# Optimization experiments

Hardware: AMD Instinct MI355X
Metric: run time of the kernel (lower is better)

## Reference

```python
import jax, jax.numpy as jnp
import numpy as np

K = 10
ALPHA = 0.1
N_NODES = 100000
N_EDGES = 1600000
D_FEAT = 50


def setup_inputs() -> dict:
    key = jax.random.key(0)
    k1, k2, k3 = jax.random.split(key, 3)
    feat = jax.random.normal(k1, (N_NODES, D_FEAT), dtype=jnp.float32)
    src = jax.random.randint(k2, (N_EDGES,), 0, N_NODES, dtype=jnp.int64)
    dst = jax.random.randint(k3, (N_EDGES,), 0, N_NODES, dtype=jnp.int64)
    return {"feat": feat, "src": src, "dst": dst}


def reference(feat, src, dst):
    # APPNP: H^{t+1} = (1-a) * D^{-1/2} A D^{-1/2} H^t + a * H^0
    n = feat.shape[0]
    # in-degree per node, clipped to >= 1 (as in the original clip_by_value)
    deg = jax.ops.segment_sum(jnp.ones(dst.shape[0], feat.dtype), dst, num_segments=n)
    norm = jnp.clip(deg, 1.0, None) ** -0.5  # [N]
    norm = norm[:, None]                      # broadcast over feature dims
    feat_0 = feat
    for _ in range(K):
        h = feat * norm                       # pre-normalize (D^{-1/2})
        # message = h[src] (edge weight is 1 since edge_drop=0), aggregate by sum at dst
        agg = jax.ops.segment_sum(h[src], dst, num_segments=n)  # [N, D]
        feat = (1.0 - ALPHA) * (agg * norm) + ALPHA * feat_0
    return feat
```

## Files before the change

kernel.cpp:

```cpp
#include <hip/hip_runtime.h>
#include <hip/hip_bf16.h>


#define NN 100000
#define EE 1600000
#define DD 50
#define GS 64
#define KK 10
#define NBLK 391

__device__ __forceinline__ float feat_at(const void* f, long long i, int ft) {
    if (ft) return ((const float*)f)[i];
    unsigned int w = ((unsigned int)((const unsigned short*)f)[i]) << 16;
    return __uint_as_float(w);
}

__device__ __forceinline__ float bf16_ld(const unsigned short* p, int i) {
    unsigned int w = ((unsigned int)p[i]) << 16;
    return __uint_as_float(w);
}

__device__ __forceinline__ unsigned short bf16_st(float x) {
    unsigned int u = __float_as_uint(x);
    unsigned int r = (u + 0x7FFF + ((u >> 16) & 1)) >> 16;
    return (unsigned short)r;
}

__global__ __launch_bounds__(512) void APPNPConv_62199716381208_kernel(
        const void* featp, const void* srcp, const void* dstp,
        int* deg, float* norm, int* row_ptr, int* col_idx, int* bsum, int* flag,
        const unsigned short* gin, unsigned short* gout, float* outp,
        int phase, int last) {
    __shared__ int sh[512];
    const int tid = threadIdx.x;
    const int gidx = blockIdx.x * blockDim.x + tid;

    if (phase == 0) {
        if (gidx < NN) deg[gidx] = 0;
        if (blockIdx.x == 0 && tid == 0) {
            const int* a = (const int*)dstp;
            int odd_or = a[1] | a[3] | a[5] | a[7] | a[9] | a[11] | a[13] | a[15];
            flag[0] = (odd_or == 0) ? 1 : 0;
            const unsigned short* w = (const unsigned short*)featp;
            int isf32 = 0;
            for (int k = 0; k < 64; ++k) {
                unsigned int b = ((unsigned int)w[k]) << 16;
                float ax = fabsf(__uint_as_float(b));
                if (!(ax < 100.0f)) isf32 = 1;
            }
            flag[1] = isf32;
        }
        return;
    }
    if (phase == 1) {
        if (gidx < EE) {
            int d = flag[0] ? (int)((const long long*)dstp)[gidx]
                            : ((const int*)dstp)[gidx];
            if ((unsigned int)d < (unsigned int)NN) atomicAdd(&deg[d], 1);
        }
        return;
    }
    if (phase == 2) {
        int i = blockIdx.x * 256 + tid;
        sh[tid] = (i < NN) ? deg[i] : 0;
        __syncthreads();
        for (int off = 128; off > 0; off >>= 1) {
            if (tid < off) sh[tid] += sh[tid + off];
            __syncthreads();
        }
        if (tid == 0) bsum[blockIdx.x] = sh[0];
        return;
    }
    if (phase == 3) {
        int v = (tid < NBLK) ? bsum[tid] : 0;
        sh[tid] = v;
        __syncthreads();
        for (int off = 1; off < 512; off <<= 1) {
            int x = (tid >= off) ? sh[tid - off] : 0;
            __syncthreads();
            sh[tid] += x;
            __syncthreads();
        }
        if (tid < NBLK) bsum[tid] = sh[tid] - v;
        return;
    }
    if (phase == 4) {
        int i = blockIdx.x * 256 + tid;
        int v = (i < NN) ? deg[i] : 0;
        sh[tid] = v;
        __syncthreads();
        for (int off = 1; off < 256; off <<= 1) {
            int x = (tid >= off) ? sh[tid - off] : 0;
            __syncthreads();
            sh[tid] += x;
            __syncthreads();
        }
        int excl = sh[tid] - v + bsum[blockIdx.x];
        if (i < NN) {
            row_ptr[i] = excl;
            deg[i] = excl;
            norm[i] = rsqrtf((float)(v < 1 ? 1 : v));
        }
        if (i == 0) row_ptr[NN] = EE;
        return;
    }
    if (phase == 5) {
        if (gidx < EE) {
            int is64 = flag[0];
            int d = is64 ? (int)((const long long*)dstp)[gidx] : ((const int*)dstp)[gidx];
            int c = is64 ? (int)((const long long*)srcp)[gidx] : ((const int*)srcp)[gidx];
            if ((unsigned int)d < (unsigned int)NN && (unsigned int)c < (unsigned int)NN) {
                int pos = atomicAdd(&deg[d], 1);
                if ((unsigned int)pos < (unsigned int)EE) col_idx[pos] = c;
            }
        }
        return;
    }
    if (phase == 6) {
        int v = gidx >> 6;
        int d = gidx & 63;
        if (v < NN && d < DD) {
            float x = feat_at(featp, (long long)v * DD + d, flag[1]);
            gout[v * GS + d] = bf16_st(x * norm[v]);
        }
        return;
    }
    {
        const int lane = tid & 63;
        const int v = (blockIdx.x << 2) + (tid >> 6);
        if (v >= NN) return;
        const int beg = row_ptr[v];
        const int end = row_ptr[v + 1];
        float s0 = 0.0f, s1 = 0.0f, s2 = 0.0f, s3 = 0.0f;
        for (int base = beg; base < end; base += 64) {
            int idx = base + lane;
            int my = (idx < end) ? col_idx[idx] : 0;
            int cnt = end - base;
            if (cnt > 64) cnt = 64;
            int j = 0;
            for (; j + 8 <= cnt; j += 8) {
                int c0 = __shfl(my, j, 64);
                int c1 = __shfl(my, j + 1, 64);
                int c2 = __shfl(my, j + 2, 64);
                int c3 = __shfl(my, j + 3, 64);
                int c4 = __shfl(my, j + 4, 64);
                int c5 = __shfl(my, j + 5, 64);
                int c6 = __shfl(my, j + 6, 64);
                int c7 = __shfl(my, j + 7, 64);
                if (lane < DD) {
                    float v0 = bf16_ld(gin, c0 * GS + lane);
                    float v1 = bf16_ld(gin, c1 * GS + lane);
                    float v2 = bf16_ld(gin, c2 * GS + lane);
                    float v3 = bf16_ld(gin, c3 * GS + lane);
                    float v4 = bf16_ld(gin, c4 * GS + lane);
                    float v5 = bf16_ld(gin, c5 * GS + lane);
                    float v6 = bf16_ld(gin, c6 * GS + lane);
                    float v7 = bf16_ld(gin, c7 * GS + lane);
                    s0 += v0 + v4;
                    s1 += v1 + v5;
                    s2 += v2 + v6;
                    s3 += v3 + v7;
                }
            }
            for (; j + 4 <= cnt; j += 4) {
                int c0 = __shfl(my, j, 64);
                int c1 = __shfl(my, j + 1, 64);
                int c2 = __shfl(my, j + 2, 64);
                int c3 = __shfl(my, j + 3, 64);
                if (lane < DD) {
                    s0 += bf16_ld(gin, c0 * GS + lane);
                    s1 += bf16_ld(gin, c1 * GS + lane);
                    s2 += bf16_ld(gin, c2 * GS + lane);
                    s3 += bf16_ld(gin, c3 * GS + lane);
                }
            }
            for (; j < cnt; ++j) {
                int c = __shfl(my, j, 64);
                if (lane < DD) s0 += bf16_ld(gin, c * GS + lane);
            }
        }
        if (lane < DD) {
            float sum = (s0 + s1) + (s2 + s3);
            float nv = norm[v];
            float f0 = feat_at(featp, (long long)v * DD + lane, flag[1]);
            float res = 0.9f * (sum * nv) + 0.1f * f0;
            if (last) outp[v * DD + lane] = res;
            else      gout[v * GS + lane] = bf16_st(res * nv);
        }
    }
}

extern "C" void kernel_launch(void* const* d_in, const int* in_sizes, int n_in,
                              void* d_out, int out_size, void* d_ws, size_t ws_size,
                              hipStream_t stream) {
    const void* featp = d_in[0];
    const void* src = d_in[1];
    const void* dst = d_in[2];
    float* outf = (float*)d_out;
    unsigned short* outb16 = (unsigned short*)d_out;
    size_t out_bytes = (size_t)out_size * 4;
    (void)in_sizes;

    if (n_in != 3) {
        hipMemsetAsync(d_out, 0x50, out_bytes, stream);
        return;
    }

    size_t a_deg  = (((size_t)NN * 4) + 255) / 256 * 256;
    size_t a_norm = a_deg;
    size_t a_rp   = (((size_t)(NN + 1) * 4) + 255) / 256 * 256;
    size_t a_col  = (((size_t)EE * 4) + 255) / 256 * 256;
    size_t a_bsum = (((size_t)NBLK * 4) + 255) / 256 * 256;
    size_t a_flag = 256;
    size_t a_buf  = (((size_t)NN * GS * 2) + 255) / 256 * 256;
    if (ws_size < a_deg + a_norm + a_rp + a_col + a_bsum + a_flag + a_buf) {
        hipMemsetAsync(d_out, 0x40, out_bytes, stream);
        return;
    }
    char* p = (char*)d_ws;
    int* deg      = (int*)p;   p += a_deg;
    float* norm   = (float*)p; p += a_norm;
    int* row_ptr  = (int*)p;   p += a_rp;
    int* col_idx  = (int*)p;   p += a_col;
    int* bsum     = (int*)p;   p += a_bsum;
    int* flag     = (int*)p;   p += a_flag;
    unsigned short* bufA = (unsigned short*)p;

    (void)hipGetLastError();

    #define LCH(grid, blk, gi, go, ph, la) \
        APPNPConv_62199716381208_kernel<<<(grid), (blk), 0, stream>>>( \
            featp, src, dst, deg, norm, row_ptr, col_idx, bsum, flag, \
            (gi), (go), outf, (ph), (la))

    LCH(NBLK, 256, bufA, bufA, 0, 0);
    LCH((EE + 255) / 256, 256, bufA, bufA, 1, 0);
    LCH(NBLK, 256, bufA, bufA, 2, 0);
    LCH(1, 512, bufA, bufA, 3, 0);
    LCH(NBLK, 256, bufA, bufA, 4, 0);
    LCH((EE + 255) / 256, 256, bufA, bufA, 5, 0);
    LCH((NN * GS + 255) / 256, 256, bufA, outb16, 6, 0);

    for (int it = 1; it <= KK; ++it) {
        const unsigned short* gi = (it & 1) ? outb16 : bufA;
        unsigned short* go       = (it & 1) ? bufA : outb16;
        LCH(NN / 4, 256, gi, go, 7, (it == KK) ? 1 : 0);
    }
    #undef LCH

    if (hipGetLastError() != hipSuccess) {
        hipMemsetAsync(d_out, 0xBF, out_bytes, stream);
    }
}
```

Baseline: 800.1 us.

## Split features into two 25-column chunks with vectorized 8-byte gathers

Splits the 50 feature columns into two independent 25-column passes, so each pass's bf16 state is 100000x32x2 bytes (about 6.4 MB), small enough to stay resident in cache during the gather. Each wavefront now processes 16 neighbors at a time, with 8 lanes each loading 4 packed bf16 values via uint2, then reduces across groups with shuffles. Non-temporal loads and stores are used for col_idx, feat and the output. In exchange, the CSR structure is traversed twice (20 gather launches instead of 10), and ping-pong buffers move from d_out into the workspace.

```diff
diff --git a/kernel.cpp b/kernel.cpp
--- a/kernel.cpp
+++ b/kernel.cpp
@@ -1,11 +1,11 @@
 #include <hip/hip_runtime.h>
-#include <hip/hip_bf16.h>
 
 
 #define NN 100000
 #define EE 1600000
 #define DD 50
-#define GS 64
+#define PS 32
+#define CF 25
 #define KK 10
 #define NBLK 391
 
@@ -15,8 +15,10 @@
     return __uint_as_float(w);
 }
 
-__device__ __forceinline__ float bf16_ld(const unsigned short* p, int i) {
-    unsigned int w = ((unsigned int)p[i]) << 16;
+__device__ __forceinline__ float feat_nt(const void* f, long long i, int ft) {
+    if (ft) return __builtin_nontemporal_load((const float*)f + i);
+    unsigned int w = ((unsigned int)__builtin_nontemporal_load(
+                         (const unsigned short*)f + i)) << 16;
     return __uint_as_float(w);
 }
 
@@ -30,7 +32,7 @@
         const void* featp, const void* srcp, const void* dstp,
         int* deg, float* norm, int* row_ptr, int* col_idx, int* bsum, int* flag,
         const unsigned short* gin, unsigned short* gout, float* outp,
-        int phase, int last) {
+        int phase, int last, int chunk) {
     __shared__ int sh[512];
     const int tid = threadIdx.x;
     const int gidx = blockIdx.x * blockDim.x + tid;
@@ -117,75 +119,94 @@
         return;
     }
     if (phase == 6) {
-        int v = gidx >> 6;
-        int d = gidx & 63;
-        if (v < NN && d < DD) {
-            float x = feat_at(featp, (long long)v * DD + d, flag[1]);
-            gout[v * GS + d] = bf16_st(x * norm[v]);
+        int v = gidx >> 5;
+        int d = gidx & 31;
+        if (v < NN) {
+            unsigned short val = 0;
+            if (d < CF) {
+                float x = feat_at(featp, (long long)v * DD + chunk * CF + d, flag[1]);
+                val = bf16_st(x * norm[v]);
+            }
+            gout[(long long)v * PS + d] = val;
         }
         return;
     }
     {
         const int lane = tid & 63;
+        const int g = lane >> 3;
+        const int s = lane & 7;
         const int v = (blockIdx.x << 2) + (tid >> 6);
         if (v >= NN) return;
         const int beg = row_ptr[v];
         const int end = row_ptr[v + 1];
-        float s0 = 0.0f, s1 = 0.0f, s2 = 0.0f, s3 = 0.0f;
+        float a0 = 0.0f, a1 = 0.0f, a2 = 0.0f, a3 = 0.0f;
         for (int base = beg; base < end; base += 64) {
             int idx = base + lane;
-            int my = (idx < end) ? col_idx[idx] : 0;
+            int my = (idx < end) ? __builtin_nontemporal_load(col_idx + idx) : 0;
             int cnt = end - base;
             if (cnt > 64) cnt = 64;
-            int j = 0;
-            for (; j + 8 <= cnt; j += 8) {
-                int c0 = __shfl(my, j, 64);
-                int c1 = __shfl(my, j + 1, 64);
-                int c2 = __shfl(my, j + 2, 64);
-                int c3 = __shfl(my, j + 3, 64);
-                int c4 = __shfl(my, j + 4, 64);
-                int c5 = __shfl(my, j + 5, 64);
-                int c6 = __shfl(my, j + 6, 64);
-                int c7 = __shfl(my, j + 7, 64);
-                if (lane < DD) {
-                    float v0 = bf16_ld(gin, c0 * GS + lane);
-                    float v1 = bf16_ld(gin, c1 * GS + lane);
-                    float v2 = bf16_ld(gin, c2 * GS + lane);
-                    float v3 = bf16_ld(gin, c3 * GS + lane);
-                    float v4 = bf16_ld(gin, c4 * GS + lane);
-                    float v5 = bf16_ld(gin, c5 * GS + lane);
-                    float v6 = bf16_ld(gin, c6 * GS + lane);
-                    float v7 = bf16_ld(gin, c7 * GS + lane);
-                    s0 += v0 + v4;
-                    s1 += v1 + v5;
-                    s2 += v2 + v6;
-                    s3 += v3 + v7;
+            for (int j = 0; j < cnt; j += 16) {
+                int ja = j + g, jb = j + 8 + g;
+                int ca = __shfl(my, ja, 64);
+                int cb = __shfl(my, jb, 64);
+                if (ja >= cnt) ca = 0;
+                if (jb >= cnt) cb = 0;
+                uint2 wa = *reinterpret_cast<const uint2*>(gin + (long long)ca * PS + s * 4);
+                uint2 wb = *reinterpret_cast<const uint2*>(gin + (long long)cb * PS + s * 4);
+                if (ja >= cnt) { wa.x = 0u; wa.y = 0u; }
+                if (jb >= cnt) { wb.x = 0u; wb.y = 0u; }
+                a0 += __uint_as_float(wa.x << 16);
+                a1 += __uint_as_float(wa.x & 0xffff0000u);
+                a2 += __uint_as_float(wa.y << 16);
+                a3 += __uint_as_float(wa.y & 0xffff0000u);
+                a0 += __uint_as_float(wb.x << 16);
+                a1 += __uint_as_float(wb.x & 0xffff0000u);
+                a2 += __uint_as_float(wb.y << 16);
+                a3 += __uint_as_float(wb.y & 0xffff0000u);
+            }
+        }
+        a0 += __shfl_xor(a0, 8, 64);  a1 += __shfl_xor(a1, 8, 64);
+        a2 += __shfl_xor(a2, 8, 64);  a3 += __shfl_xor(a3, 8, 64);
+        a0 += __shfl_xor(a0, 16, 64); a1 += __shfl_xor(a1, 16, 64);
+        a2 += __shfl_xor(a2, 16, 64); a3 += __shfl_xor(a3, 16, 64);
+        a0 += __shfl_xor(a0, 32, 64); a1 += __shfl_xor(a1, 32, 64);
+        a2 += __shfl_xor(a2, 32, 64); a3 += __shfl_xor(a3, 32, 64);
+        if (g == 0) {
+            const float nv = norm[v];
+            const int ft = flag[1];
+            float acc[4] = {a0, a1, a2, a3};
+            if (last) {
+                #pragma unroll
+                for (int k = 0; k < 4; ++k) {
+                    int e = s * 4 + k;
+                    if (e < CF) {
+                        long long fi = (long long)v * DD + chunk * CF + e;
+                        float f0 = feat_nt(featp, fi, ft);
+                        outp[fi] = 0.9f * (acc[k] * nv) + 0.1f * f0;
+                    }
                 }
-            }
-            for (; j + 4 <= cnt; j += 4) {
-                int c0 = __shfl(my, j, 64);
-                int c1 = __shfl(my, j + 1, 64);
-                int c2 = __shfl(my, j + 2, 64);
-                int c3 = __shfl(my, j + 3, 64);
-                if (lane < DD) {
-                    s0 += bf16_ld(gin, c0 * GS + lane);
-                    s1 += bf16_ld(gin, c1 * GS + lane);
-                    s2 += bf16_ld(gin, c2 * GS + lane);
-                    s3 += bf16_ld(gin, c3 * GS + lane);
+            } else {
+                unsigned short h[4];
+                #pragma unroll
+                for (int k = 0; k < 4; ++k) {
+                    int e = s * 4 + k;
+                    if (e < CF) {
+                        long long fi = (long long)v * DD + chunk * CF + e;
+                        float f0 = feat_nt(featp, fi, ft);
+                        float res = 0.9f * (acc[k] * nv) + 0.1f * f0;
+                        h[k] = bf16_st(res * nv);
+                    } else {
+                        h[k] = 0;
+                    }
                 }
-            }
-            for (; j < cnt; ++j) {
-                int c = __shfl(my, j, 64);
-                if (lane < DD) s0 += bf16_ld(gin, c * GS + lane);
-            }
-        }
-        if (lane < DD) {
-            float sum = (s0 + s1) + (s2 + s3);
-            float nv = norm[v];
-            float f0 = feat_at(featp, (long long)v * DD + lane, flag[1]);
-            float res = 0.9f * (sum * nv) + 0.1f * f0;
-            if (last) outp[v * DD + lane] = res;
-            else      gout[v * GS + lane] = bf16_st(res * nv);
+                unsigned long long pk =
+                    (unsigned long long)h[0]
+                    | ((unsigned long long)h[1] << 16)
+                    | ((unsigned long long)h[2] << 32)
+                    | ((unsigned long long)h[3] << 48);
+                __builtin_nontemporal_store(pk,
+                    reinterpret_cast<unsigned long long*>(gout + (long long)v * PS + s * 4));
+            }
         }
     }
 }
@@ -197,7 +218,6 @@
     const void* src = d_in[1];
     const void* dst = d_in[2];
     float* outf = (float*)d_out;
-    unsigned short* outb16 = (unsigned short*)d_out;
     size_t out_bytes = (size_t)out_size * 4;
     (void)in_sizes;
 
@@ -212,8 +232,8 @@
     size_t a_col  = (((size_t)EE * 4) + 255) / 256 * 256;
     size_t a_bsum = (((size_t)NBLK * 4) + 255) / 256 * 256;
     size_t a_flag = 256;
-    size_t a_buf  = (((size_t)NN * GS * 2) + 255) / 256 * 256;
-    if (ws_size < a_deg + a_norm + a_rp + a_col + a_bsum + a_flag + a_buf) {
+    size_t a_buf  = (((size_t)NN * PS * 2) + 255) / 256 * 256;
+    if (ws_size < a_deg + a_norm + a_rp + a_col + a_bsum + a_flag + 2 * a_buf) {
         hipMemsetAsync(d_out, 0x40, out_bytes, stream);
         return;
     }
@@ -224,27 +244,30 @@
     int* col_idx  = (int*)p;   p += a_col;
     int* bsum     = (int*)p;   p += a_bsum;
     int* flag     = (int*)p;   p += a_flag;
-    unsigned short* bufA = (unsigned short*)p;
+    unsigned short* P0 = (unsigned short*)p; p += a_buf;
+    unsigned short* P1 = (unsigned short*)p;
 
     (void)hipGetLastError();
 
-    #define LCH(grid, blk, gi, go, ph, la) \
+    #define LCH(grid, blk, gi, go, ph, la, ch) \
         APPNPConv_62199716381208_kernel<<<(grid), (blk), 0, stream>>>( \
             featp, src, dst, deg, norm, row_ptr, col_idx, bsum, flag, \
-            (gi), (go), outf, (ph), (la))
-
-    LCH(NBLK, 256, bufA, bufA, 0, 0);
-    LCH((EE + 255) / 256, 256, bufA, bufA, 1, 0);
-    LCH(NBLK, 256, bufA, bufA, 2, 0);
-    LCH(1, 512, bufA, bufA, 3, 0);
-    LCH(NBLK, 256, bufA, bufA, 4, 0);
-    LCH((EE + 255) / 256, 256, bufA, bufA, 5, 0);
-    LCH((NN * GS + 255) / 256, 256, bufA, outb16, 6, 0);
-
-    for (int it = 1; it <= KK; ++it) {
-        const unsigned short* gi = (it & 1) ? outb16 : bufA;
-        unsigned short* go       = (it & 1) ? bufA : outb16;
-        LCH(NN / 4, 256, gi, go, 7, (it == KK) ? 1 : 0);
+            (gi), (go), outf, (ph), (la), (ch))
+
+    LCH(NBLK, 256, P0, P0, 0, 0, 0);
+    LCH((EE + 255) / 256, 256, P0, P0, 1, 0, 0);
+    LCH(NBLK, 256, P0, P0, 2, 0, 0);
+    LCH(1, 512, P0, P0, 3, 0, 0);
+    LCH(NBLK, 256, P0, P0, 4, 0, 0);
+    LCH((EE + 255) / 256, 256, P0, P0, 5, 0, 0);
+
+    for (int c = 0; c < 2; ++c) {
+        LCH((NN * PS) / 256, 256, P0, P0, 6, 0, c);
+        for (int it = 1; it <= KK; ++it) {
+            const unsigned short* gi = (it & 1) ? P0 : P1;
+            unsigned short* go       = (it & 1) ? P1 : P0;
+            LCH(NN / 4, 256, gi, go, 7, (it == KK) ? 1 : 0, c);
+        }
     }
     #undef LCH
 
```

Result: slower. 1.531 ms (+91.4%).

## Build CSR via per-slice shared-memory histograms instead of global atomics

Applied to the files above, without the earlier changes.

Replaces the global-atomic degree count and scatter with a two-pass, shared-memory counting sort. Edges are split into 32 slices and destinations into 8 ranges, giving 256 blocks that each keep a 12500-entry LDS histogram. Per-slice counts are kept in the output buffer as scratch, and prefix offsets are computed per slice so each block scatters through LDS atomics. The aim is to remove contended global atomics in CSR construction. The cost is that every block rereads its whole edge slice once per range (8x edge reads), and within-node column order becomes deterministic by slice.

```diff
diff --git a/kernel.cpp b/kernel.cpp
--- a/kernel.cpp
+++ b/kernel.cpp
@@ -1,5 +1,4 @@
 #include <hip/hip_runtime.h>
-#include <hip/hip_bf16.h>
 
 
 #define NN 100000
@@ -8,6 +7,10 @@
 #define GS 64
 #define KK 10
 #define NBLK 391
+#define SLICES 32
+#define RANGES 8
+#define NR (NN / RANGES)
+#define ES (EE / SLICES)
 
 __device__ __forceinline__ float feat_at(const void* f, long long i, int ft) {
     if (ft) return ((const float*)f)[i];
@@ -26,17 +29,60 @@
     return (unsigned short)r;
 }
 
+__global__ __launch_bounds__(512) void APPNPConv_62199716381208_build(
+        const void* srcp, const void* dstp, unsigned int* counts,
+        int* col_idx, const int* flag, int phase) {
+    __shared__ unsigned int hist[NR];
+    const int tid = threadIdx.x;
+    const int r = blockIdx.x / SLICES;
+    const int s = blockIdx.x % SLICES;
+    const int r0 = r * NR;
+    const int is64 = flag[0];
+    const int e0 = s * ES;
+
+    if (phase == 0) {
+        for (int i = tid; i < NR; i += 512) hist[i] = 0u;
+        __syncthreads();
+        for (int i = tid; i < ES; i += 512) {
+            int e = e0 + i;
+            int d = is64 ? (int)((const long long*)dstp)[e]
+                         : ((const int*)dstp)[e];
+            unsigned int dr = (unsigned int)(d - r0);
+            if (dr < (unsigned int)NR) atomicAdd(&hist[dr], 1u);
+        }
+        __syncthreads();
+        for (int i = tid; i < NR; i += 512)
+            counts[(size_t)s * NN + r0 + i] = hist[i];
+    } else {
+        for (int i = tid; i < NR; i += 512)
+            hist[i] = counts[(size_t)s * NN + r0 + i];
+        __syncthreads();
+        for (int i = tid; i < ES; i += 512) {
+            int e = e0 + i;
+            int d = is64 ? (int)((const long long*)dstp)[e]
+                         : ((const int*)dstp)[e];
+            int c = is64 ? (int)((const long long*)srcp)[e]
+                         : ((const int*)srcp)[e];
+            unsigned int dr = (unsigned int)(d - r0);
+            if (dr < (unsigned int)NR) {
+                unsigned int pos = atomicAdd(&hist[dr], 1u);
+                if (pos < (unsigned int)EE)
+                    col_idx[pos] = ((unsigned int)c < (unsigned int)NN) ? c : 0;
+            }
+        }
+    }
+}
+
 __global__ __launch_bounds__(512) void APPNPConv_62199716381208_kernel(
         const void* featp, const void* srcp, const void* dstp,
         int* deg, float* norm, int* row_ptr, int* col_idx, int* bsum, int* flag,
+        unsigned int* counts,
         const unsigned short* gin, unsigned short* gout, float* outp,
         int phase, int last) {
     __shared__ int sh[512];
     const int tid = threadIdx.x;
-    const int gidx = blockIdx.x * blockDim.x + tid;
 
     if (phase == 0) {
-        if (gidx < NN) deg[gidx] = 0;
         if (blockIdx.x == 0 && tid == 0) {
             const int* a = (const int*)dstp;
             int odd_or = a[1] | a[3] | a[5] | a[7] | a[9] | a[11] | a[13] | a[15];
@@ -52,17 +98,17 @@
         }
         return;
     }
-    if (phase == 1) {
-        if (gidx < EE) {
-            int d = flag[0] ? (int)((const long long*)dstp)[gidx]
-                            : ((const int*)dstp)[gidx];
-            if ((unsigned int)d < (unsigned int)NN) atomicAdd(&deg[d], 1);
-        }
-        return;
-    }
     if (phase == 2) {
-        int i = blockIdx.x * 256 + tid;
-        sh[tid] = (i < NN) ? deg[i] : 0;
+        int n = blockIdx.x * 256 + tid;
+        int total = 0;
+        if (n < NN) {
+            #pragma unroll 4
+            for (int s = 0; s < SLICES; ++s)
+                total += (int)counts[(size_t)s * NN + n];
+            deg[n] = total;
+            norm[n] = rsqrtf((float)(total < 1 ? 1 : total));
+        }
+        sh[tid] = total;
         __syncthreads();
         for (int off = 128; off > 0; off >>= 1) {
             if (tid < off) sh[tid] += sh[tid + off];
@@ -98,25 +144,19 @@
         int excl = sh[tid] - v + bsum[blockIdx.x];
         if (i < NN) {
             row_ptr[i] = excl;
-            deg[i] = excl;
-            norm[i] = rsqrtf((float)(v < 1 ? 1 : v));
+            unsigned int run = (unsigned int)excl;
+            for (int s = 0; s < SLICES; ++s) {
+                size_t o = (size_t)s * NN + i;
+                unsigned int c = counts[o];
+                counts[o] = run;
+                run += c;
+            }
         }
         if (i == 0) row_ptr[NN] = EE;
         return;
     }
-    if (phase == 5) {
-        if (gidx < EE) {
-            int is64 = flag[0];
-            int d = is64 ? (int)((const long long*)dstp)[gidx] : ((const int*)dstp)[gidx];
-            int c = is64 ? (int)((const long long*)srcp)[gidx] : ((const int*)srcp)[gidx];
-            if ((unsigned int)d < (unsigned int)NN && (unsigned int)c < (unsigned int)NN) {
-                int pos = atomicAdd(&deg[d], 1);
-                if ((unsigned int)pos < (unsigned int)EE) col_idx[pos] = c;
-            }
-        }
-        return;
-    }
     if (phase == 6) {
+        int gidx = blockIdx.x * 256 + tid;
         int v = gidx >> 6;
         int d = gidx & 63;
         if (v < NN && d < DD) {
@@ -198,6 +238,7 @@
     const void* dst = d_in[2];
     float* outf = (float*)d_out;
     unsigned short* outb16 = (unsigned short*)d_out;
+    unsigned int* counts = (unsigned int*)d_out;
     size_t out_bytes = (size_t)out_size * 4;
     (void)in_sizes;
 
@@ -213,7 +254,8 @@
     size_t a_bsum = (((size_t)NBLK * 4) + 255) / 256 * 256;
     size_t a_flag = 256;
     size_t a_buf  = (((size_t)NN * GS * 2) + 255) / 256 * 256;
-    if (ws_size < a_deg + a_norm + a_rp + a_col + a_bsum + a_flag + a_buf) {
+    if (ws_size < a_deg + a_norm + a_rp + a_col + a_bsum + a_flag + a_buf ||
+        out_bytes < (size_t)SLICES * NN * 4) {
         hipMemsetAsync(d_out, 0x40, out_bytes, stream);
         return;
     }
@@ -230,15 +272,18 @@
 
     #define LCH(grid, blk, gi, go, ph, la) \
         APPNPConv_62199716381208_kernel<<<(grid), (blk), 0, stream>>>( \
-            featp, src, dst, deg, norm, row_ptr, col_idx, bsum, flag, \
+            featp, src, dst, deg, norm, row_ptr, col_idx, bsum, flag, counts, \
             (gi), (go), outf, (ph), (la))
-
-    LCH(NBLK, 256, bufA, bufA, 0, 0);
-    LCH((EE + 255) / 256, 256, bufA, bufA, 1, 0);
+    #define LCB(ph) \
+        APPNPConv_62199716381208_build<<<SLICES * RANGES, 512, 0, stream>>>( \
+            src, dst, counts, col_idx, flag, (ph))
+
+    LCH(1, 256, bufA, bufA, 0, 0);
+    LCB(0);
     LCH(NBLK, 256, bufA, bufA, 2, 0);
     LCH(1, 512, bufA, bufA, 3, 0);
     LCH(NBLK, 256, bufA, bufA, 4, 0);
-    LCH((EE + 255) / 256, 256, bufA, bufA, 5, 0);
+    LCB(1);
     LCH((NN * GS + 255) / 256, 256, bufA, outb16, 6, 0);
 
     for (int it = 1; it <= KK; ++it) {
@@ -247,6 +292,7 @@
         LCH(NN / 4, 256, gi, go, 7, (it == KK) ? 1 : 0);
     }
     #undef LCH
+    #undef LCB
 
     if (hipGetLastError() != hipSuccess) {
         hipMemsetAsync(d_out, 0xBF, out_bytes, stream);
```

Measured after the change: 724.9 us. 1.1x faster.
